# Optimization experiments

Hardware: AMD Instinct MI355X
Metric: run time of the kernel (lower is better)

The kernel has to match this reference:

```python
import jax, jax.numpy as jnp
import numpy as np

B, S, D, H = 4, 2048, 1024, 16
HD = D // H


def sinusoidal_pe(max_len, d_model):
    pos = np.arange(max_len)[:, None].astype(np.float32)
    div = np.exp(np.arange(0, d_model, 2).astype(np.float32) * (-np.log(10000.0) / d_model))
    pe = np.zeros((max_len, d_model), dtype=np.float32)
    pe[:, 0::2] = np.sin(pos * div)
    pe[:, 1::2] = np.cos(pos * div)
    return jnp.asarray(pe)


def setup_inputs() -> dict:
    key = jax.random.key(0)
    ks = jax.random.split(key, 9)
    s = 1.0 / np.sqrt(D)
    inp = {
        "x": jax.random.normal(ks[0], (B, S, D), dtype=jnp.float32),
        "Wq": jax.random.normal(ks[1], (D, D), dtype=jnp.float32) * s,
        "bq": jnp.zeros((D,), dtype=jnp.float32),
        "Wk": jax.random.normal(ks[2], (D, D), dtype=jnp.float32) * s,
        "bk": jnp.zeros((D,), dtype=jnp.float32),
        "Wv": jax.random.normal(ks[3], (D, D), dtype=jnp.float32) * s,
        "bv": jnp.zeros((D,), dtype=jnp.float32),
        "Wp": jax.random.normal(ks[4], (D, D), dtype=jnp.float32) * s,
        "bp": jnp.zeros((D,), dtype=jnp.float32),
        "pe": sinusoidal_pe(S, D),
    }
    return inp


def reference(x, Wq, bq, Wk, bk, Wv, bv, Wp, bp, pe):
    # positional encoding (eval mode: dropout is identity)
    xp = x + pe[None, :, :]  # [B,S,D]
    split = lambda t: t.reshape(B, S, H, HD).transpose(0, 2, 1, 3)  # [B,H,S,HD]
    q = split(xp @ Wq.T + bq)
    k = split(xp @ Wk.T + bk)
    v = split(xp @ Wv.T + bv)
    scores = jnp.einsum("bhqd,bhkd->bhqk", q, k) / jnp.sqrt(jnp.float32(HD))
    attn = jax.nn.softmax(scores, axis=-1)
    ctx = jnp.einsum("bhqk,bhkd->bhqd", attn, v)
    ctx = ctx.transpose(0, 2, 1, 3).reshape(B, S, D)
    return ctx @ Wp.T + bp
```

## Files before the change

### kernel.cpp

```cpp
#include <hip/hip_runtime.h>
#include <hip/hip_bf16.h>
#include <stdint.h>

#define B_  4
#define S_  2048
#define D_  1024
#define H_  16
#define HD_ 64

typedef __bf16 bfx8   __attribute__((ext_vector_type(8)));
typedef float  f32x4  __attribute__((ext_vector_type(4)));
typedef float  f32x16 __attribute__((ext_vector_type(16)));
typedef short  s16x4  __attribute__((ext_vector_type(4)));
typedef float  fl4    __attribute__((ext_vector_type(4)));
typedef unsigned int u32x2 __attribute__((ext_vector_type(2)));
typedef unsigned int u32x4 __attribute__((ext_vector_type(4)));

#define EXP2(x) __builtin_amdgcn_exp2f(x)

static __device__ __forceinline__ unsigned short f2bf(float f) {
    union { float f; unsigned int u; } v; v.f = f;
    unsigned int r = v.u + 0x7fffu + ((v.u >> 16) & 1u);
    return (unsigned short)(r >> 16);
}
static __device__ __forceinline__ unsigned int fbits(float f) {
    union { float f; unsigned int u; } v; v.f = f; return v.u;
}

#define GLD_LDS16(gp, lp) __builtin_amdgcn_global_load_lds( \
    (const __attribute__((address_space(1))) unsigned int*)(gp), \
    (__attribute__((address_space(3))) unsigned int*)(lp), 16, 0, 0)

__global__ __launch_bounds__(256) void xpe_kernel(
    const float* __restrict__ x, const float* __restrict__ pe,
    unsigned short* __restrict__ xpb)
{
    int i = (blockIdx.x * 256 + threadIdx.x) * 4;
    fl4 xv = *(const fl4*)(x + i);
    fl4 pv = *(const fl4*)(pe + (i & (S_ * D_ - 1)));
    s16x4 r;
#pragma unroll
    for (int j = 0; j < 4; j++) r[j] = (short)f2bf(xv[j] + pv[j]);
    *(s16x4*)(xpb + i) = r;
}

__global__ __launch_bounds__(256) void cvt4_kernel(
    const float* __restrict__ w0, const float* __restrict__ w1,
    const float* __restrict__ w2, const float* __restrict__ w3,
    unsigned short* __restrict__ o)
{
    int blk = blockIdx.x;
    int wsel = blk >> 10;
    const float* src = wsel == 0 ? w0 : wsel == 1 ? w1 : wsel == 2 ? w2 : w3;
    int i = (((blk & 1023) * 256) + threadIdx.x) * 4;
    fl4 v = *(const fl4*)(src + i);
    s16x4 r;
#pragma unroll
    for (int j = 0; j < 4; j++) r[j] = (short)f2bf(v[j]);
    *(s16x4*)(o + (size_t)wsel * D_ * D_ + i) = r;
}

template<int MODE>
__global__ __launch_bounds__(256, 2) void gemm_bt(
    const unsigned short* __restrict__ A,
    const unsigned short* __restrict__ Bw,
    const float* __restrict__ bias,
    void* __restrict__ Cout, float oscale)
{
    constexpr int K = D_;
    constexpr int N = D_;
    __shared__ unsigned short As[128 * 32];
    __shared__ unsigned short Bs[128 * 32];
    const int hw = blockIdx.x;
    const int logical = (hw & 7) * 64 + (hw >> 3);
    const int m0 = (logical >> 3) * 128;
    const int n0 = (logical & 7) * 128;

    const int t  = threadIdx.x;
    const int l  = t & 63;
    const int w  = t >> 6;
    const int wr = (w >> 1) * 64;
    const int wc = (w & 1) * 64;
    const int lr = l & 15;
    const int lg = l >> 4;
    const int lk = lg * 8;

    const int e0 = t * 8;
    const int sr = e0 >> 5;
    const int sc = e0 & 31;
    const unsigned short* pA = A  + (size_t)(m0 + sr) * K + sc;
    const unsigned short* pB = Bw + (size_t)(n0 + sr) * K + sc;

    f32x4 acc[4][4] = {};

    for (int k0 = 0; k0 < K; k0 += 32) {
        __syncthreads();
        GLD_LDS16(pA + k0,                    As + e0);
        GLD_LDS16(pA + k0 + (size_t)64 * K,   As + 2048 + e0);
        GLD_LDS16(pB + k0,                    Bs + e0);
        GLD_LDS16(pB + k0 + (size_t)64 * K,   Bs + 2048 + e0);
        __syncthreads();
        bfx8 af[4], bf[4];
#pragma unroll
        for (int i = 0; i < 4; i++)
            af[i] = *(const bfx8*)(As + (wr + i * 16 + lr) * 32 + lk);
#pragma unroll
        for (int i = 0; i < 4; i++)
            bf[i] = *(const bfx8*)(Bs + (wc + i * 16 + lr) * 32 + lk);
#pragma unroll
        for (int i = 0; i < 4; i++)
#pragma unroll
            for (int j = 0; j < 4; j++)
                acc[i][j] = __builtin_amdgcn_mfma_f32_16x16x32_bf16(
                    af[i], bf[j], acc[i][j], 0, 0, 0);
    }

#pragma unroll
    for (int i = 0; i < 4; i++) {
        const int row0 = m0 + wr + i * 16 + lg * 4;
#pragma unroll
        for (int j = 0; j < 4; j++) {
            const int col = n0 + wc + j * 16 + lr;
            const float bv = bias[col];
            if (MODE == 0) {
                unsigned short* C = (unsigned short*)Cout;
#pragma unroll
                for (int v = 0; v < 4; v++)
                    C[(size_t)(row0 + v) * N + col] = f2bf((acc[i][j][v] + bv) * oscale);
            } else if (MODE == 1) {
                unsigned short* C = (unsigned short*)Cout;
                const int bidx = row0 >> 11;
                const int s0   = row0 & (S_ - 1);
                s16x4 r;
#pragma unroll
                for (int v = 0; v < 4; v++) r[v] = (short)f2bf(acc[i][j][v] + bv);
                *(s16x4*)(C + (size_t)(bidx * D_ + col) * S_ + s0) = r;
            } else {
                float* C = (float*)Cout;
#pragma unroll
                for (int v = 0; v < 4; v++)
                    C[(size_t)(row0 + v) * N + col] = acc[i][j][v] + bv;
            }
        }
    }
}

__global__ __launch_bounds__(256, 4) void attn_kernel(
    const unsigned short* __restrict__ Qb,
    const unsigned short* __restrict__ Kb,
    const unsigned short* __restrict__ Vt,
    unsigned short* __restrict__ Ctx)
{
    __shared__ __align__(16) unsigned short Ks[2][64 * 64];
    __shared__ __align__(16) unsigned short Vs[2][64 * 64];

    const int hw = blockIdx.x;
    const int logical = (hw & 7) * 128 + (hw >> 3);
    const int bh = logical >> 4;
    const int t  = threadIdx.x;
    const int l  = t & 63;
    const int w  = t >> 6;
    const int b  = bh >> 4;
    const int h  = bh & 15;
    const int lr = l & 31;
    const int hi = l >> 5;
    const int q0 = (logical & 15) * 128 + w * 32;

    const unsigned short* Qbase = Qb + (size_t)b * S_ * D_ + h * HD_;
    const unsigned short* Kbase = Kb + (size_t)b * S_ * D_ + h * HD_;
    const unsigned short* Vbase = Vt + (size_t)bh * HD_ * S_;

    const int r0  = t >> 3;
    const int cgs = (t & 7) ^ (r0 & 7);
    const unsigned short* Ksrc0 = Kbase + (size_t)r0 * D_ + cgs * 8;
    const unsigned short* Ksrc1 = Kbase + (size_t)(r0 + 32) * D_ + cgs * 8;
    const unsigned short* Vsrc0 = Vbase + (size_t)r0 * S_ + cgs * 8;
    const unsigned short* Vsrc1 = Vbase + (size_t)(r0 + 32) * S_ + cgs * 8;
    const int ld0 = t * 8, ld1 = t * 8 + 2048;

    GLD_LDS16(Ksrc0, &Ks[0][ld0]);
    GLD_LDS16(Ksrc1, &Ks[0][ld1]);
    GLD_LDS16(Vsrc0, &Vs[0][ld0]);
    GLD_LDS16(Vsrc1, &Vs[0][ld1]);

    bfx8 qf[4];
#pragma unroll
    for (int t4 = 0; t4 < 4; t4++)
        qf[t4] = *(const bfx8*)(Qbase + (size_t)(q0 + lr) * D_ + t4 * 16 + hi * 8);

    f32x16 acc0 = {}, acc1 = {};
    float l_r = 0.f;
    const int sw = lr & 7;

    int cur = 0;
    for (int ki = 0; ki < S_ / 64; ki++) {
        __syncthreads();
        if (ki + 1 < S_ / 64) {
            GLD_LDS16(Ksrc0 + (size_t)(ki + 1) * 64 * D_, &Ks[cur ^ 1][ld0]);
            GLD_LDS16(Ksrc1 + (size_t)(ki + 1) * 64 * D_, &Ks[cur ^ 1][ld1]);
            GLD_LDS16(Vsrc0 + (ki + 1) * 64,              &Vs[cur ^ 1][ld0]);
            GLD_LDS16(Vsrc1 + (ki + 1) * 64,              &Vs[cur ^ 1][ld1]);
        }
        const unsigned short* Kc = Ks[cur];
        const unsigned short* Vc = Vs[cur];

        f32x16 s0 = {}, s1 = {};
#pragma unroll
        for (int t4 = 0; t4 < 4; t4++) {
            const int ch = ((t4 * 2 + hi) ^ sw) * 8;
            bfx8 a0 = *(const bfx8*)(Kc + lr * 64 + ch);
            bfx8 a1 = *(const bfx8*)(Kc + (32 + lr) * 64 + ch);
            s0 = __builtin_amdgcn_mfma_f32_32x32x16_bf16(a0, qf[t4], s0, 0, 0, 0);
            s1 = __builtin_amdgcn_mfma_f32_32x32x16_bf16(a1, qf[t4], s1, 0, 0, 0);
        }

        float c0 = 0.f, c1 = 0.f, c2 = 0.f, c3 = 0.f;
#pragma unroll
        for (int r = 0; r < 16; r += 4) {
            float p0 = EXP2(s0[r]);     s0[r] = p0;     c0 += p0;
            float p1 = EXP2(s0[r + 1]); s0[r + 1] = p1; c1 += p1;
            float p2 = EXP2(s0[r + 2]); s0[r + 2] = p2; c2 += p2;
            float p3 = EXP2(s0[r + 3]); s0[r + 3] = p3; c3 += p3;
        }
#pragma unroll
        for (int r = 0; r < 16; r += 4) {
            float p0 = EXP2(s1[r]);     s1[r] = p0;     c0 += p0;
            float p1 = EXP2(s1[r + 1]); s1[r + 1] = p1; c1 += p1;
            float p2 = EXP2(s1[r + 2]); s1[r + 2] = p2; c2 += p2;
            float p3 = EXP2(s1[r + 3]); s1[r + 3] = p3; c3 += p3;
        }
        l_r += (c0 + c1) + (c2 + c3);

        unsigned pk0[8], pk1[8];
#pragma unroll
        for (int i = 0; i < 8; i++) {
            pk0[i] = __builtin_amdgcn_perm(fbits(s0[2 * i + 1]), fbits(s0[2 * i]), 0x07060302u);
            pk1[i] = __builtin_amdgcn_perm(fbits(s1[2 * i + 1]), fbits(s1[2 * i]), 0x07060302u);
        }

#pragma unroll
        for (int ks = 0; ks < 4; ks++) {
            const int c = (ks & 1) * 4;
            const unsigned pa0 = (ks >> 1) ? pk1[c]     : pk0[c];
            const unsigned pa1 = (ks >> 1) ? pk1[c + 1] : pk0[c + 1];
            const unsigned pa2 = (ks >> 1) ? pk1[c + 2] : pk0[c + 2];
            const unsigned pa3 = (ks >> 1) ? pk1[c + 3] : pk0[c + 3];
            u32x2 r02 = __builtin_amdgcn_permlane32_swap(pa0, pa2, false, false);
            u32x2 r13 = __builtin_amdgcn_permlane32_swap(pa1, pa3, false, false);
            u32x4 bfr;
            bfr[0] = r02[0];
            bfr[1] = r13[0];
            bfr[2] = r02[1];
            bfr[3] = r13[1];
            union { u32x4 u; bfx8 b; } cvt; cvt.u = bfr;

            const int ch = ((ks * 2 + hi) ^ sw) * 8;
            bfx8 v0 = *(const bfx8*)(Vc + lr * 64 + ch);
            bfx8 v1 = *(const bfx8*)(Vc + (32 + lr) * 64 + ch);
            acc0 = __builtin_amdgcn_mfma_f32_32x32x16_bf16(v0, cvt.b, acc0, 0, 0, 0);
            acc1 = __builtin_amdgcn_mfma_f32_32x32x16_bf16(v1, cvt.b, acc1, 0, 0, 0);
        }
        cur ^= 1;
    }

    const float l_tot = l_r + __shfl_xor(l_r, 32);
    const float rinv = 1.0f / l_tot;
    unsigned short* Cb = Ctx + (size_t)b * S_ * D_ + (size_t)(q0 + lr) * D_ + h * HD_;
#pragma unroll
    for (int dt = 0; dt < 2; dt++)
#pragma unroll
        for (int a = 0; a < 4; a++) {
            s16x4 rv;
#pragma unroll
            for (int v = 0; v < 4; v++)
                rv[v] = (short)f2bf((dt ? acc1[4 * a + v] : acc0[4 * a + v]) * rinv);
            *(s16x4*)(Cb + dt * 32 + 8 * a + 4 * hi) = rv;
        }
}

extern "C" void kernel_launch(void* const* d_in, const int* in_sizes, int n_in,
                              void* d_out, int out_size, void* d_ws, size_t ws_size,
                              hipStream_t stream)
{
    const float* x  = (const float*)d_in[0];
    const float* Wq = (const float*)d_in[1];
    const float* bq = (const float*)d_in[2];
    const float* Wk = (const float*)d_in[3];
    const float* bk = (const float*)d_in[4];
    const float* Wv = (const float*)d_in[5];
    const float* bv = (const float*)d_in[6];
    const float* Wp = (const float*)d_in[7];
    const float* bp = (const float*)d_in[8];
    const float* pe = (const float*)d_in[9];

    char* ws = (char*)d_ws;
    const size_t MD = (size_t)B_ * S_ * D_;
    unsigned short* xpb = (unsigned short*)ws; ws += MD * 2;
    unsigned short* wqb = (unsigned short*)ws; ws += (size_t)D_ * D_ * 2;
    unsigned short* wkb = (unsigned short*)ws; ws += (size_t)D_ * D_ * 2;
    unsigned short* wvb = (unsigned short*)ws; ws += (size_t)D_ * D_ * 2;
    unsigned short* wpb = (unsigned short*)ws; ws += (size_t)D_ * D_ * 2;
    unsigned short* qb  = (unsigned short*)ws; ws += MD * 2;
    unsigned short* kb  = (unsigned short*)ws; ws += MD * 2;
    unsigned short* vtb = (unsigned short*)ws; ws += MD * 2;
    unsigned short* ctb = (unsigned short*)ws; ws += MD * 2;

    xpe_kernel<<<(int)(MD / (256 * 4)), 256, 0, stream>>>(x, pe, xpb);
    cvt4_kernel<<<4096, 256, 0, stream>>>(Wq, Wk, Wv, Wp, wqb);

    const float qscale = 0.125f * 1.44269504088896340736f;

    gemm_bt<0><<<512, 256, 0, stream>>>(xpb, wqb, bq, qb,  qscale);
    gemm_bt<0><<<512, 256, 0, stream>>>(xpb, wkb, bk, kb,  1.0f);
    gemm_bt<1><<<512, 256, 0, stream>>>(xpb, wvb, bv, vtb, 1.0f);

    attn_kernel<<<1024, 256, 0, stream>>>(qb, kb, vtb, ctb);

    gemm_bt<2><<<512, 256, 0, stream>>>(ctb, wpb, bp, d_out, 1.0f);
}
```

Baseline: 211.2 us.

## Fuse QKV projections into one GEMM launch, merge prep kernels, add MFMA priority

Merges the x+pe conversion and the weight conversion into one launch. Replaces three separate Q/K/V GEMM launches with a single 1536-block GEMM over the concatenated weights, picking bias, scale and output layout per column block and mapping blocks so each XCD shares A rows. Adds s_setprio around the MFMA sections in attention to favour matrix issue. This cuts launch overhead and tail effects between the small kernels, at the cost of a runtime branch in the epilogue.

```diff
diff --git a/kernel.cpp b/kernel.cpp
--- a/kernel.cpp
+++ b/kernel.cpp
@@ -31,41 +31,124 @@
     (const __attribute__((address_space(1))) unsigned int*)(gp), \
     (__attribute__((address_space(3))) unsigned int*)(lp), 16, 0, 0)
 
-__global__ __launch_bounds__(256) void xpe_kernel(
+__global__ __launch_bounds__(256) void prep_kernel(
     const float* __restrict__ x, const float* __restrict__ pe,
-    unsigned short* __restrict__ xpb)
-{
-    int i = (blockIdx.x * 256 + threadIdx.x) * 4;
-    fl4 xv = *(const fl4*)(x + i);
-    fl4 pv = *(const fl4*)(pe + (i & (S_ * D_ - 1)));
-    s16x4 r;
-#pragma unroll
-    for (int j = 0; j < 4; j++) r[j] = (short)f2bf(xv[j] + pv[j]);
-    *(s16x4*)(xpb + i) = r;
-}
-
-__global__ __launch_bounds__(256) void cvt4_kernel(
     const float* __restrict__ w0, const float* __restrict__ w1,
     const float* __restrict__ w2, const float* __restrict__ w3,
-    unsigned short* __restrict__ o)
-{
-    int blk = blockIdx.x;
-    int wsel = blk >> 10;
-    const float* src = wsel == 0 ? w0 : wsel == 1 ? w1 : wsel == 2 ? w2 : w3;
-    int i = (((blk & 1023) * 256) + threadIdx.x) * 4;
-    fl4 v = *(const fl4*)(src + i);
-    s16x4 r;
-#pragma unroll
-    for (int j = 0; j < 4; j++) r[j] = (short)f2bf(v[j]);
-    *(s16x4*)(o + (size_t)wsel * D_ * D_ + i) = r;
-}
-
-template<int MODE>
-__global__ __launch_bounds__(256, 2) void gemm_bt(
+    unsigned short* __restrict__ xpb, unsigned short* __restrict__ wcat)
+{
+    const int blk = blockIdx.x;
+    if (blk < 8192) {
+        int i = (blk * 256 + threadIdx.x) * 4;
+        fl4 xv = *(const fl4*)(x + i);
+        fl4 pv = *(const fl4*)(pe + (i & (S_ * D_ - 1)));
+        s16x4 r;
+#pragma unroll
+        for (int j = 0; j < 4; j++) r[j] = (short)f2bf(xv[j] + pv[j]);
+        *(s16x4*)(xpb + i) = r;
+    } else {
+        const int bb = blk - 8192;
+        const int wsel = bb >> 10;
+        const float* src = wsel == 0 ? w0 : wsel == 1 ? w1 : wsel == 2 ? w2 : w3;
+        int i = (((bb & 1023) * 256) + threadIdx.x) * 4;
+        fl4 v = *(const fl4*)(src + i);
+        s16x4 r;
+#pragma unroll
+        for (int j = 0; j < 4; j++) r[j] = (short)f2bf(v[j]);
+        *(s16x4*)(wcat + (size_t)wsel * D_ * D_ + i) = r;
+    }
+}
+
+__global__ __launch_bounds__(256, 2) void gemm_qkv(
+    const unsigned short* __restrict__ A,
+    const unsigned short* __restrict__ Bw,
+    const float* __restrict__ bq, const float* __restrict__ bk,
+    const float* __restrict__ bv,
+    unsigned short* __restrict__ Qo, unsigned short* __restrict__ Ko,
+    unsigned short* __restrict__ Vo, float qscale)
+{
+    constexpr int K = D_;
+    __shared__ unsigned short As[128 * 32];
+    __shared__ unsigned short Bs[128 * 32];
+    const int hw  = blockIdx.x;
+    const int xcd = hw & 7;
+    const int i_  = hw >> 3;
+    const int m0  = (i_ / 3) * 128;
+    const int n0  = (xcd * 3 + i_ % 3) * 128;
+
+    const int t  = threadIdx.x;
+    const int l  = t & 63;
+    const int w  = t >> 6;
+    const int wr = (w >> 1) * 64;
+    const int wc = (w & 1) * 64;
+    const int lr = l & 15;
+    const int lg = l >> 4;
+    const int lk = lg * 8;
+
+    const int e0 = t * 8;
+    const int sr = e0 >> 5;
+    const int sc = e0 & 31;
+    const unsigned short* pA = A  + (size_t)(m0 + sr) * K + sc;
+    const unsigned short* pB = Bw + (size_t)(n0 + sr) * K + sc;
+
+    f32x4 acc[4][4] = {};
+
+    for (int k0 = 0; k0 < K; k0 += 32) {
+        __syncthreads();
+        GLD_LDS16(pA + k0,                    As + e0);
+        GLD_LDS16(pA + k0 + (size_t)64 * K,   As + 2048 + e0);
+        GLD_LDS16(pB + k0,                    Bs + e0);
+        GLD_LDS16(pB + k0 + (size_t)64 * K,   Bs + 2048 + e0);
+        __syncthreads();
+        bfx8 af[4], bf[4];
+#pragma unroll
+        for (int i = 0; i < 4; i++)
+            af[i] = *(const bfx8*)(As + (wr + i * 16 + lr) * 32 + lk);
+#pragma unroll
+        for (int i = 0; i < 4; i++)
+            bf[i] = *(const bfx8*)(Bs + (wc + i * 16 + lr) * 32 + lk);
+#pragma unroll
+        for (int i = 0; i < 4; i++)
+#pragma unroll
+            for (int j = 0; j < 4; j++)
+                acc[i][j] = __builtin_amdgcn_mfma_f32_16x16x32_bf16(
+                    af[i], bf[j], acc[i][j], 0, 0, 0);
+    }
+
+    const int sel = n0 >> 10;
+    const float* bias = sel == 0 ? bq : sel == 1 ? bk : bv;
+    const float osc = sel == 0 ? qscale : 1.0f;
+
+#pragma unroll
+    for (int i = 0; i < 4; i++) {
+        const int row0 = m0 + wr + i * 16 + lg * 4;
+#pragma unroll
+        for (int j = 0; j < 4; j++) {
+            const int colf = n0 + wc + j * 16 + lr;
+            const int ocol = colf & 1023;
+            const float bvv = bias[ocol];
+            if (sel < 2) {
+                unsigned short* C = sel == 0 ? Qo : Ko;
+#pragma unroll
+                for (int v = 0; v < 4; v++)
+                    C[(size_t)(row0 + v) * D_ + ocol] = f2bf((acc[i][j][v] + bvv) * osc);
+            } else {
+                const int bidx = row0 >> 11;
+                const int s0   = row0 & (S_ - 1);
+                s16x4 r;
+#pragma unroll
+                for (int v = 0; v < 4; v++) r[v] = (short)f2bf(acc[i][j][v] + bvv);
+                *(s16x4*)(Vo + (size_t)(bidx * D_ + ocol) * S_ + s0) = r;
+            }
+        }
+    }
+}
+
+__global__ __launch_bounds__(256, 2) void gemm_out(
     const unsigned short* __restrict__ A,
     const unsigned short* __restrict__ Bw,
     const float* __restrict__ bias,
-    void* __restrict__ Cout, float oscale)
+    float* __restrict__ Cout)
 {
     constexpr int K = D_;
     constexpr int N = D_;
@@ -122,25 +205,9 @@
         for (int j = 0; j < 4; j++) {
             const int col = n0 + wc + j * 16 + lr;
             const float bv = bias[col];
-            if (MODE == 0) {
-                unsigned short* C = (unsigned short*)Cout;
-#pragma unroll
-                for (int v = 0; v < 4; v++)
-                    C[(size_t)(row0 + v) * N + col] = f2bf((acc[i][j][v] + bv) * oscale);
-            } else if (MODE == 1) {
-                unsigned short* C = (unsigned short*)Cout;
-                const int bidx = row0 >> 11;
-                const int s0   = row0 & (S_ - 1);
-                s16x4 r;
-#pragma unroll
-                for (int v = 0; v < 4; v++) r[v] = (short)f2bf(acc[i][j][v] + bv);
-                *(s16x4*)(C + (size_t)(bidx * D_ + col) * S_ + s0) = r;
-            } else {
-                float* C = (float*)Cout;
-#pragma unroll
-                for (int v = 0; v < 4; v++)
-                    C[(size_t)(row0 + v) * N + col] = acc[i][j][v] + bv;
-            }
+#pragma unroll
+            for (int v = 0; v < 4; v++)
+                Cout[(size_t)(row0 + v) * N + col] = acc[i][j][v] + bv;
         }
     }
 }
@@ -205,6 +272,7 @@
         const unsigned short* Vc = Vs[cur];
 
         f32x16 s0 = {}, s1 = {};
+        __builtin_amdgcn_s_setprio(1);
 #pragma unroll
         for (int t4 = 0; t4 < 4; t4++) {
             const int ch = ((t4 * 2 + hi) ^ sw) * 8;
@@ -213,6 +281,7 @@
             s0 = __builtin_amdgcn_mfma_f32_32x32x16_bf16(a0, qf[t4], s0, 0, 0, 0);
             s1 = __builtin_amdgcn_mfma_f32_32x32x16_bf16(a1, qf[t4], s1, 0, 0, 0);
         }
+        __builtin_amdgcn_s_setprio(0);
 
         float c0 = 0.f, c1 = 0.f, c2 = 0.f, c3 = 0.f;
 #pragma unroll
@@ -257,8 +326,10 @@
             const int ch = ((ks * 2 + hi) ^ sw) * 8;
             bfx8 v0 = *(const bfx8*)(Vc + lr * 64 + ch);
             bfx8 v1 = *(const bfx8*)(Vc + (32 + lr) * 64 + ch);
+            __builtin_amdgcn_s_setprio(1);
             acc0 = __builtin_amdgcn_mfma_f32_32x32x16_bf16(v0, cvt.b, acc0, 0, 0, 0);
             acc1 = __builtin_amdgcn_mfma_f32_32x32x16_bf16(v1, cvt.b, acc1, 0, 0, 0);
+            __builtin_amdgcn_s_setprio(0);
         }
         cur ^= 1;
     }
@@ -305,16 +376,13 @@
     unsigned short* vtb = (unsigned short*)ws; ws += MD * 2;
     unsigned short* ctb = (unsigned short*)ws; ws += MD * 2;
 
-    xpe_kernel<<<(int)(MD / (256 * 4)), 256, 0, stream>>>(x, pe, xpb);
-    cvt4_kernel<<<4096, 256, 0, stream>>>(Wq, Wk, Wv, Wp, wqb);
+    prep_kernel<<<12288, 256, 0, stream>>>(x, pe, Wq, Wk, Wv, Wp, xpb, wqb);
 
     const float qscale = 0.125f * 1.44269504088896340736f;
 
-    gemm_bt<0><<<512, 256, 0, stream>>>(xpb, wqb, bq, qb,  qscale);
-    gemm_bt<0><<<512, 256, 0, stream>>>(xpb, wkb, bk, kb,  1.0f);
-    gemm_bt<1><<<512, 256, 0, stream>>>(xpb, wvb, bv, vtb, 1.0f);
+    gemm_qkv<<<1536, 256, 0, stream>>>(xpb, wqb, bq, bk, bv, qb, kb, vtb, qscale);
 
     attn_kernel<<<1024, 256, 0, stream>>>(qb, kb, vtb, ctb);
 
-    gemm_bt<2><<<512, 256, 0, stream>>>(ctb, wpb, bp, d_out, 1.0f);
-}
+    gemm_out<<<512, 256, 0, stream>>>(ctb, wpb, bp, (float*)d_out);
+}
```

New measurement: 201.8 us. -4.4%, faster.
